# Optimization experiments

Hardware: AMD Instinct MI355X
Metric: run time of the kernel (lower is better)

## Reference

```python
import jax, jax.numpy as jnp
import numpy as np

N_NODES = 50000
N_EDGES = 800000
N_FEAT = 128
DIM = 32
N_GRAPHS = 500
N_CLASSES = 2


def setup_inputs() -> dict:
    key = jax.random.key(0)
    ks = jax.random.split(key, 10)
    x = jax.random.normal(ks[0], (N_NODES, N_FEAT), dtype=jnp.float32)
    edge_index = jax.random.randint(ks[1], (2, N_EDGES), 0, N_NODES, dtype=jnp.int64)
    batch = jnp.sort(jax.random.randint(ks[2], (N_NODES,), 0, N_GRAPHS, dtype=jnp.int64))
    edge_weight = jax.random.uniform(ks[3], (N_EDGES,), dtype=jnp.float32)
    s = 1.0 / np.sqrt(N_FEAT)
    w_rel = jax.random.uniform(ks[4], (N_FEAT, DIM), jnp.float32, -s, s)
    b_rel = jax.random.uniform(ks[5], (DIM,), jnp.float32, -s, s)
    w_root = jax.random.uniform(ks[6], (N_FEAT, DIM), jnp.float32, -s, s)
    s2 = 1.0 / np.sqrt(DIM)
    w_fc1 = jax.random.uniform(ks[7], (DIM, DIM), jnp.float32, -s2, s2)
    b_fc1 = jnp.zeros((DIM,), jnp.float32)
    w_fc2 = jax.random.uniform(ks[8], (DIM, N_CLASSES), jnp.float32, -s2, s2)
    b_fc2 = jnp.zeros((N_CLASSES,), jnp.float32)
    return {"x": x, "edge_weight": edge_weight, "w_rel": w_rel, "b_rel": b_rel,
            "w_root": w_root, "w_fc1": w_fc1, "b_fc1": b_fc1, "w_fc2": w_fc2,
            "b_fc2": b_fc2, "edge_index": edge_index, "batch": batch}


def reference(x, edge_weight, w_rel, b_rel, w_root, w_fc1, b_fc1, w_fc2, b_fc2,
              edge_index, batch):
    src, dst = edge_index[0], edge_index[1]
    # GraphConv: out_i = lin_rel(sum_{j->i} w_ji * x_j) + lin_root(x_i)
    msg = x[src] * edge_weight[:, None]                      # [E, F]
    agg = jax.ops.segment_sum(msg, dst, num_segments=N_NODES)  # [N, F]
    h = agg @ w_rel + b_rel + x @ w_root                     # [N, DIM]
    h = jax.nn.relu(h)
    # global_add_pool over graph ids
    pooled = jax.ops.segment_sum(h, batch, num_segments=N_GRAPHS)  # [G, DIM]
    h2 = jax.nn.relu(pooled @ w_fc1 + b_fc1)
    # dropout is identity in eval mode
    logits = h2 @ w_fc2 + b_fc2
    return jax.nn.log_softmax(logits, axis=-1)
```

## Files before the change

### kernel.cpp

```cpp
#include <hip/hip_runtime.h>

#define NN 50000
#define NE 800000
#define NF 128
#define DIM 32
#define NG 500
#define BK 32
#define NB ((NN + BK - 1) / BK)
#define PB 782
#define HB 128
#define CHUNK_E ((NE + HB - 1) / HB)
#define CAP 1024
#define SC7 7

typedef float  f32x4  __attribute__((ext_vector_type(4)));
typedef __bf16 bf16x8 __attribute__((ext_vector_type(8)));
typedef unsigned short u16x8 __attribute__((ext_vector_type(8)));

__device__ __forceinline__ unsigned rne16(float f) {
    unsigned u = __float_as_uint(f);
    return (u + 0x7FFFu + ((u >> 16) & 1u)) >> 16;
}
#define UIF __uint_as_float
__device__ __forceinline__ float blo(unsigned p) { return UIF(p << 16); }
__device__ __forceinline__ float bhi(unsigned p) { return UIF(p & 0xFFFF0000u); }

__global__ __launch_bounds__(256) void projhist_kernel(
    const float* __restrict__ x, const float* __restrict__ w_rel,
    const float* __restrict__ w_root, const float* __restrict__ b_rel,
    unsigned* __restrict__ yp, unsigned* __restrict__ rootp,
    const int* __restrict__ ei, int* __restrict__ H, float* __restrict__ pooled)
{
    __shared__ unsigned short s_wb[64 * 136];
    __shared__ float s_out[64 * 65];
    int tid = threadIdx.x;

    if (blockIdx.x >= PB) {
        int blk = blockIdx.x - PB;
        int* sh = (int*)s_wb;
        int pi = blk * 256 + tid;
        if (pi < NG * DIM) pooled[pi] = 0.0f;
        for (int i = tid; i < NB; i += 256) sh[i] = 0;
        __syncthreads();
        int base = blk * CHUNK_E;
        int end  = min(base + CHUNK_E, NE);
        for (int e = base + tid; e < end; e += 256)
            atomicAdd(&sh[ei[NE + e] >> 5], 1);
        __syncthreads();
        for (int i = tid; i < NB; i += 256) H[blk * NB + i] = sh[i];
        return;
    }

    for (int i = tid; i < 64 * NF; i += 256) {
        int k   = i >> 6;
        int col = i & 63;
        float v = (col < DIM) ? w_rel[k * DIM + col] : w_root[k * DIM + (col - DIM)];
        s_wb[col * 136 + k] = (unsigned short)rne16(v);
    }
    int rb = blockIdx.x * 64;
    __syncthreads();

    int l    = tid & 63;
    int w    = tid >> 6;
    int mrow = l & 15;
    int q    = l >> 4;
    int arow = min(rb + w * 16 + mrow, NN - 1);
    const float* xr = x + (size_t)arow * NF + q * 8;

    f32x4 acc0 = {0,0,0,0}, acc1 = {0,0,0,0}, acc2 = {0,0,0,0}, acc3 = {0,0,0,0};
#pragma unroll
    for (int k0 = 0; k0 < NF; k0 += 32) {
        float4 xa = *reinterpret_cast<const float4*>(xr + k0);
        float4 xb = *reinterpret_cast<const float4*>(xr + k0 + 4);
        u16x8 au;
        au[0] = (unsigned short)rne16(xa.x); au[1] = (unsigned short)rne16(xa.y);
        au[2] = (unsigned short)rne16(xa.z); au[3] = (unsigned short)rne16(xa.w);
        au[4] = (unsigned short)rne16(xb.x); au[5] = (unsigned short)rne16(xb.y);
        au[6] = (unsigned short)rne16(xb.z); au[7] = (unsigned short)rne16(xb.w);
        bf16x8 a = __builtin_bit_cast(bf16x8, au);
        int kb = k0 + q * 8;
        bf16x8 b0 = *reinterpret_cast<const bf16x8*>(&s_wb[(0  + mrow) * 136 + kb]);
        bf16x8 b1 = *reinterpret_cast<const bf16x8*>(&s_wb[(16 + mrow) * 136 + kb]);
        bf16x8 b2 = *reinterpret_cast<const bf16x8*>(&s_wb[(32 + mrow) * 136 + kb]);
        bf16x8 b3 = *reinterpret_cast<const bf16x8*>(&s_wb[(48 + mrow) * 136 + kb]);
        acc0 = __builtin_amdgcn_mfma_f32_16x16x32_bf16(a, b0, acc0, 0, 0, 0);
        acc1 = __builtin_amdgcn_mfma_f32_16x16x32_bf16(a, b1, acc1, 0, 0, 0);
        acc2 = __builtin_amdgcn_mfma_f32_16x16x32_bf16(a, b2, acc2, 0, 0, 0);
        acc3 = __builtin_amdgcn_mfma_f32_16x16x32_bf16(a, b3, acc3, 0, 0, 0);
    }
#pragma unroll
    for (int reg = 0; reg < 4; ++reg) {
        int srow = w * 16 + q * 4 + reg;
        s_out[srow * 65 +  0 + mrow] = acc0[reg];
        s_out[srow * 65 + 16 + mrow] = acc1[reg];
        s_out[srow * 65 + 32 + mrow] = acc2[reg];
        s_out[srow * 65 + 48 + mrow] = acc3[reg];
    }
    __syncthreads();

#pragma unroll
    for (int rep = 0; rep < 8; ++rep) {
        int idx = tid + rep * 256;
        int row = idx >> 5;
        int ui  = idx & 31;
        int n   = rb + row;
        if (n < NN) {
            if (ui < 16) {
                int c0 = ui * 2;
                unsigned p = rne16(s_out[row * 65 + c0]) |
                             (rne16(s_out[row * 65 + c0 + 1]) << 16);
                yp[(size_t)n * 16 + ui] = p;
            } else {
                int c0 = (ui - 16) * 2;
                float f0 = s_out[row * 65 + DIM + c0]     + b_rel[c0];
                float f1 = s_out[row * 65 + DIM + c0 + 1] + b_rel[c0 + 1];
                rootp[(size_t)n * 16 + (ui - 16)] = rne16(f0) | (rne16(f1) << 16);
            }
        }
    }
}

__global__ __launch_bounds__(256) void colscan(
    int* __restrict__ H, int* __restrict__ colsum)
{
    int b = blockIdx.x * 256 + threadIdx.x;
    if (b >= NB) return;
    int run = 0;
#pragma unroll 8
    for (int blk = 0; blk < HB; ++blk) {
        int v = H[blk * NB + b];
        H[blk * NB + b] = run;
        run += v;
    }
    colsum[b] = run;
}

__global__ __launch_bounds__(256) void partition_kernel(
    const int* __restrict__ ei, const float* __restrict__ ew,
    const int* __restrict__ H, const int* __restrict__ colsum,
    uint2* __restrict__ part, int* __restrict__ boff)
{
    __shared__ int s_scan[256];
    __shared__ int s_boff[NB + 1];
    __shared__ int cur[NB];
    int t = threadIdx.x;
    {
        int v[SC7]; int sum = 0;
#pragma unroll
        for (int j = 0; j < SC7; ++j) {
            int idx = t * SC7 + j;
            v[j] = (idx < NB) ? colsum[idx] : 0;
            sum += v[j];
        }
        s_scan[t] = sum;
        __syncthreads();
        for (int o = 1; o < 256; o <<= 1) {
            int u = (t >= o) ? s_scan[t - o] : 0;
            __syncthreads();
            s_scan[t] += u;
            __syncthreads();
        }
        int b2 = s_scan[t] - sum;
#pragma unroll
        for (int j = 0; j < SC7; ++j) {
            int idx = t * SC7 + j;
            if (idx < NB) { s_boff[idx] = b2; b2 += v[j]; }
        }
        if (t == 0) s_boff[NB] = NE;
        __syncthreads();
    }
    if (blockIdx.x == 0)
        for (int i = t; i <= NB; i += 256) boff[i] = s_boff[i];

    for (int i = t; i < NB; i += 256)
        cur[i] = s_boff[i] + H[blockIdx.x * NB + i];
    __syncthreads();
    int base = blockIdx.x * CHUNK_E;
    int end  = min(base + CHUNK_E, NE);
    for (int e = base + t; e < end; e += 256) {
        int s = ei[e], d = ei[NE + e];
        float w = ew[e];
        int b = d >> 5;
        int pos = atomicAdd(&cur[b], 1);
        part[pos] = make_uint2((unsigned)s | ((unsigned)(d & 31) << 16),
                               __float_as_uint(w));
    }
}

__global__ __launch_bounds__(256) void bucketagg_kernel(
    const uint2* __restrict__ ypq, const uint2* __restrict__ rootq,
    const uint2* __restrict__ part, const int* __restrict__ boff,
    const int* __restrict__ batch, float* __restrict__ pooled)
{
    __shared__ unsigned csr_lds[CAP];
    __shared__ int cnt[BK];
    __shared__ int cur[BK];
    __shared__ int off[BK + 1];
    int b = blockIdx.x, t = threadIdx.x;
    int s0 = boff[b], s1 = boff[b + 1], m = s1 - s0;

    uint2 rec[4];
    int nrec = 0;
    if (t < BK) cnt[t] = 0;
    __syncthreads();
#pragma unroll
    for (int i = 0; i < 4; ++i) {
        int idx = t + i * 256;
        if (idx < m) { rec[i] = part[s0 + idx]; nrec = i + 1; }
    }
#pragma unroll
    for (int i = 0; i < 4; ++i)
        if (i < nrec) atomicAdd(&cnt[rec[i].x >> 16], 1);
    __syncthreads();
    if (t < BK) {
        int v = cnt[t];
        int inc = v;
#pragma unroll
        for (int o = 1; o < BK; o <<= 1) {
            int u = __shfl_up(inc, o, 64);
            if (t >= o) inc += u;
        }
        off[t] = inc - v;
        cur[t] = inc - v;
        if (t == BK - 1) off[BK] = inc;
    }
    __syncthreads();
#pragma unroll
    for (int i = 0; i < 4; ++i)
        if (i < nrec) {
            uint2 pk = rec[i];
            int nl = pk.x >> 16;
            int pos = atomicAdd(&cur[nl], 1);
            csr_lds[pos] = (pk.x & 0xFFFFu) | (rne16(UIF(pk.y)) << 16);
        }
    if (t < BK) {
        int n = b * BK + t;
        cnt[t] = (n < NN) ? batch[n] : -1;
    }
    __syncthreads();

    int w    = t >> 6;
    int lane = t & 63;
    int g    = lane >> 3;
    int j    = lane & 7;
    int nl   = w * 8 + g;
    int n    = b * BK + nl;
    float v0 = 0, v1 = 0, v2 = 0, v3 = 0;
    if (n < NN) {
        int e  = off[nl];
        int e1 = off[nl + 1];
        for (; e + 4 <= e1; e += 4) {
            unsigned c0 = csr_lds[e],     c1 = csr_lds[e + 1];
            unsigned c2 = csr_lds[e + 2], c3 = csr_lds[e + 3];
            uint2 p0 = ypq[(c0 & 0xFFFFu) * 8 + j];
            uint2 p1 = ypq[(c1 & 0xFFFFu) * 8 + j];
            uint2 p2 = ypq[(c2 & 0xFFFFu) * 8 + j];
            uint2 p3 = ypq[(c3 & 0xFFFFu) * 8 + j];
            float w0 = UIF(c0 & 0xFFFF0000u), w1 = UIF(c1 & 0xFFFF0000u);
            float w2 = UIF(c2 & 0xFFFF0000u), w3 = UIF(c3 & 0xFFFF0000u);
            v0 = fmaf(w0, blo(p0.x), v0); v1 = fmaf(w0, bhi(p0.x), v1);
            v2 = fmaf(w0, blo(p0.y), v2); v3 = fmaf(w0, bhi(p0.y), v3);
            v0 = fmaf(w1, blo(p1.x), v0); v1 = fmaf(w1, bhi(p1.x), v1);
            v2 = fmaf(w1, blo(p1.y), v2); v3 = fmaf(w1, bhi(p1.y), v3);
            v0 = fmaf(w2, blo(p2.x), v0); v1 = fmaf(w2, bhi(p2.x), v1);
            v2 = fmaf(w2, blo(p2.y), v2); v3 = fmaf(w2, bhi(p2.y), v3);
            v0 = fmaf(w3, blo(p3.x), v0); v1 = fmaf(w3, bhi(p3.x), v1);
            v2 = fmaf(w3, blo(p3.y), v2); v3 = fmaf(w3, bhi(p3.y), v3);
        }
        for (; e < e1; ++e) {
            unsigned cu = csr_lds[e];
            uint2 p = ypq[(cu & 0xFFFFu) * 8 + j];
            float ww = UIF(cu & 0xFFFF0000u);
            v0 = fmaf(ww, blo(p.x), v0); v1 = fmaf(ww, bhi(p.x), v1);
            v2 = fmaf(ww, blo(p.y), v2); v3 = fmaf(ww, bhi(p.y), v3);
        }
        uint2 rr = rootq[(size_t)n * 8 + j];
        v0 = fmaxf(v0 + blo(rr.x), 0.0f);
        v1 = fmaxf(v1 + bhi(rr.x), 0.0f);
        v2 = fmaxf(v2 + blo(rr.y), 0.0f);
        v3 = fmaxf(v3 + bhi(rr.y), 0.0f);
    }
    __syncthreads();

    float* s_p = (float*)csr_lds;
    {
        float* dst = s_p + nl * DIM + 4 * j;
        dst[0] = v0; dst[1] = v1; dst[2] = v2; dst[3] = v3;
    }
    __syncthreads();

    int gi = t >> 5, c = t & 31;
    int rung = -1; float run = 0.0f;
#pragma unroll
    for (int k = 0; k < 4; ++k) {
        int nl2 = gi * 4 + k;
        int n2  = b * BK + nl2;
        if (n2 >= NN) break;
        float v = s_p[nl2 * DIM + c];
        int gg = cnt[nl2];
        if (gg != rung) {
            if (rung >= 0) atomicAdd(&pooled[rung * DIM + c], run);
            rung = gg; run = v;
        } else run += v;
    }
    if (rung >= 0) atomicAdd(&pooled[rung * DIM + c], run);
}

__global__ __launch_bounds__(512) void head_kernel(
    const float* __restrict__ pooled, const float* __restrict__ w_fc1,
    const float* __restrict__ b_fc1, const float* __restrict__ w_fc2,
    const float* __restrict__ b_fc2, float* __restrict__ out)
{
    __shared__ float s_fc1[DIM * DIM];
    __shared__ float s_b1[DIM];
    __shared__ float s_fc2[DIM * 2];
    __shared__ float s_b2[2];
    int tid = threadIdx.x;
    s_fc1[tid]       = w_fc1[tid];
    s_fc1[tid + 512] = w_fc1[tid + 512];
    if (tid < DIM * 2) s_fc2[tid] = w_fc2[tid];
    if (tid < DIM)     s_b1[tid]  = b_fc1[tid];
    if (tid < 2)       s_b2[tid]  = b_fc2[tid];
    __syncthreads();

    int g = tid;
    if (g >= NG) return;
    const float* p = pooled + g * DIM;
    float h2[DIM];
#pragma unroll
    for (int c = 0; c < DIM; ++c) {
        float a = s_b1[c];
#pragma unroll
        for (int k = 0; k < DIM; ++k)
            a = fmaf(p[k], s_fc1[k * DIM + c], a);
        h2[c] = a > 0.0f ? a : 0.0f;
    }
    float l0 = s_b2[0], l1 = s_b2[1];
#pragma unroll
    for (int c = 0; c < DIM; ++c) {
        l0 = fmaf(h2[c], s_fc2[c * 2 + 0], l0);
        l1 = fmaf(h2[c], s_fc2[c * 2 + 1], l1);
    }
    float m   = fmaxf(l0, l1);
    float lse = m + logf(expf(l0 - m) + expf(l1 - m));
    out[g * 2 + 0] = l0 - lse;
    out[g * 2 + 1] = l1 - lse;
}

extern "C" void kernel_launch(void* const* d_in, const int* in_sizes, int n_in,
                              void* d_out, int out_size, void* d_ws, size_t ws_size,
                              hipStream_t stream) {
    const float* x      = (const float*)d_in[0];
    const float* ew     = (const float*)d_in[1];
    const float* w_rel  = (const float*)d_in[2];
    const float* b_rel  = (const float*)d_in[3];
    const float* w_root = (const float*)d_in[4];
    const float* w_fc1  = (const float*)d_in[5];
    const float* b_fc1  = (const float*)d_in[6];
    const float* w_fc2  = (const float*)d_in[7];
    const float* b_fc2  = (const float*)d_in[8];
    const int*   ei     = (const int*)d_in[9];
    const int*   batch  = (const int*)d_in[10];
    float* out = (float*)d_out;

    char* ws = (char*)d_ws;
    unsigned* yp    = (unsigned*)ws;
    unsigned* rootp = yp + (size_t)NN * 16;
    uint2* part     = (uint2*)(rootp + (size_t)NN * 16);
    int*   H        = (int*)(part + NE);
    int*   colsum   = H + (size_t)HB * NB;
    int*   boff     = colsum + NB;
    float* pooled   = (float*)(boff + NB + 2);

    projhist_kernel<<<PB + HB, 256, 0, stream>>>(x, w_rel, w_root, b_rel,
                                                 yp, rootp, ei, H, pooled);
    colscan<<<(NB + 255) / 256, 256, 0, stream>>>(H, colsum);
    partition_kernel<<<HB, 256, 0, stream>>>(ei, ew, H, colsum, part, boff);
    bucketagg_kernel<<<NB, 256, 0, stream>>>((const uint2*)yp, (const uint2*)rootp,
                                             part, boff, batch, pooled);
    head_kernel<<<1, 512, 0, stream>>>(pooled, w_fc1, b_fc1, w_fc2, b_fc2, out);
}
```

Measured before the change: 66.99 us.

## Fuse MLP head into bucket aggregation via last-block ticket; unroll gather by 8

Removes the separate head kernel launch. The last bucketagg block to finish, found with an atomic ticket counter that projhist resets, now runs the FC1/FC2/log-softmax head after a threadfence, staging the head weights in an enlarged LDS buffer. The edge gather loop is also unrolled from 4 to 8 to keep more independent loads in flight. The costs are a serialized tail on one 256-thread block, higher LDS and register use, and reliance on the threadfence/ticket pattern for correct ordering of the atomics.

```diff
diff --git a/kernel.cpp b/kernel.cpp
--- a/kernel.cpp
+++ b/kernel.cpp
@@ -11,6 +11,7 @@
 #define HB 128
 #define CHUNK_E ((NE + HB - 1) / HB)
 #define CAP 1024
+#define LDSW 1184
 #define SC7 7
 
 typedef float  f32x4  __attribute__((ext_vector_type(4)));
@@ -29,7 +30,8 @@
     const float* __restrict__ x, const float* __restrict__ w_rel,
     const float* __restrict__ w_root, const float* __restrict__ b_rel,
     unsigned* __restrict__ yp, unsigned* __restrict__ rootp,
-    const int* __restrict__ ei, int* __restrict__ H, float* __restrict__ pooled)
+    const int* __restrict__ ei, int* __restrict__ H, float* __restrict__ pooled,
+    int* __restrict__ done_cnt)
 {
     __shared__ unsigned short s_wb[64 * 136];
     __shared__ float s_out[64 * 65];
@@ -38,6 +40,7 @@
     if (blockIdx.x >= PB) {
         int blk = blockIdx.x - PB;
         int* sh = (int*)s_wb;
+        if (blk == 0 && tid == 0) *done_cnt = 0;
         int pi = blk * 256 + tid;
         if (pi < NG * DIM) pooled[pi] = 0.0f;
         for (int i = tid; i < NB; i += 256) sh[i] = 0;
@@ -190,12 +193,17 @@
 __global__ __launch_bounds__(256) void bucketagg_kernel(
     const uint2* __restrict__ ypq, const uint2* __restrict__ rootq,
     const uint2* __restrict__ part, const int* __restrict__ boff,
-    const int* __restrict__ batch, float* __restrict__ pooled)
+    const int* __restrict__ batch, float* __restrict__ pooled,
+    int* __restrict__ done_cnt,
+    const float* __restrict__ w_fc1, const float* __restrict__ b_fc1,
+    const float* __restrict__ w_fc2, const float* __restrict__ b_fc2,
+    float* __restrict__ out)
 {
-    __shared__ unsigned csr_lds[CAP];
+    __shared__ unsigned csr_lds[LDSW];
     __shared__ int cnt[BK];
     __shared__ int cur[BK];
     __shared__ int off[BK + 1];
+    __shared__ int s_last;
     int b = blockIdx.x, t = threadIdx.x;
     int s0 = boff[b], s1 = boff[b + 1], m = s1 - s0;
 
@@ -249,15 +257,23 @@
     if (n < NN) {
         int e  = off[nl];
         int e1 = off[nl + 1];
-        for (; e + 4 <= e1; e += 4) {
+        for (; e + 8 <= e1; e += 8) {
             unsigned c0 = csr_lds[e],     c1 = csr_lds[e + 1];
             unsigned c2 = csr_lds[e + 2], c3 = csr_lds[e + 3];
+            unsigned c4 = csr_lds[e + 4], c5 = csr_lds[e + 5];
+            unsigned c6 = csr_lds[e + 6], c7 = csr_lds[e + 7];
             uint2 p0 = ypq[(c0 & 0xFFFFu) * 8 + j];
             uint2 p1 = ypq[(c1 & 0xFFFFu) * 8 + j];
             uint2 p2 = ypq[(c2 & 0xFFFFu) * 8 + j];
             uint2 p3 = ypq[(c3 & 0xFFFFu) * 8 + j];
+            uint2 p4 = ypq[(c4 & 0xFFFFu) * 8 + j];
+            uint2 p5 = ypq[(c5 & 0xFFFFu) * 8 + j];
+            uint2 p6 = ypq[(c6 & 0xFFFFu) * 8 + j];
+            uint2 p7 = ypq[(c7 & 0xFFFFu) * 8 + j];
             float w0 = UIF(c0 & 0xFFFF0000u), w1 = UIF(c1 & 0xFFFF0000u);
             float w2 = UIF(c2 & 0xFFFF0000u), w3 = UIF(c3 & 0xFFFF0000u);
+            float w4 = UIF(c4 & 0xFFFF0000u), w5 = UIF(c5 & 0xFFFF0000u);
+            float w6 = UIF(c6 & 0xFFFF0000u), w7 = UIF(c7 & 0xFFFF0000u);
             v0 = fmaf(w0, blo(p0.x), v0); v1 = fmaf(w0, bhi(p0.x), v1);
             v2 = fmaf(w0, blo(p0.y), v2); v3 = fmaf(w0, bhi(p0.y), v3);
             v0 = fmaf(w1, blo(p1.x), v0); v1 = fmaf(w1, bhi(p1.x), v1);
@@ -266,6 +282,14 @@
             v2 = fmaf(w2, blo(p2.y), v2); v3 = fmaf(w2, bhi(p2.y), v3);
             v0 = fmaf(w3, blo(p3.x), v0); v1 = fmaf(w3, bhi(p3.x), v1);
             v2 = fmaf(w3, blo(p3.y), v2); v3 = fmaf(w3, bhi(p3.y), v3);
+            v0 = fmaf(w4, blo(p4.x), v0); v1 = fmaf(w4, bhi(p4.x), v1);
+            v2 = fmaf(w4, blo(p4.y), v2); v3 = fmaf(w4, bhi(p4.y), v3);
+            v0 = fmaf(w5, blo(p5.x), v0); v1 = fmaf(w5, bhi(p5.x), v1);
+            v2 = fmaf(w5, blo(p5.y), v2); v3 = fmaf(w5, bhi(p5.y), v3);
+            v0 = fmaf(w6, blo(p6.x), v0); v1 = fmaf(w6, bhi(p6.x), v1);
+            v2 = fmaf(w6, blo(p6.y), v2); v3 = fmaf(w6, bhi(p6.y), v3);
+            v0 = fmaf(w7, blo(p7.x), v0); v1 = fmaf(w7, bhi(p7.x), v1);
+            v2 = fmaf(w7, blo(p7.y), v2); v3 = fmaf(w7, bhi(p7.y), v3);
         }
         for (; e < e1; ++e) {
             unsigned cu = csr_lds[e];
@@ -304,47 +328,46 @@
         } else run += v;
     }
     if (rung >= 0) atomicAdd(&pooled[rung * DIM + c], run);
-}
-
-__global__ __launch_bounds__(512) void head_kernel(
-    const float* __restrict__ pooled, const float* __restrict__ w_fc1,
-    const float* __restrict__ b_fc1, const float* __restrict__ w_fc2,
-    const float* __restrict__ b_fc2, float* __restrict__ out)
-{
-    __shared__ float s_fc1[DIM * DIM];
-    __shared__ float s_b1[DIM];
-    __shared__ float s_fc2[DIM * 2];
-    __shared__ float s_b2[2];
-    int tid = threadIdx.x;
-    s_fc1[tid]       = w_fc1[tid];
-    s_fc1[tid + 512] = w_fc1[tid + 512];
-    if (tid < DIM * 2) s_fc2[tid] = w_fc2[tid];
-    if (tid < DIM)     s_b1[tid]  = b_fc1[tid];
-    if (tid < 2)       s_b2[tid]  = b_fc2[tid];
-    __syncthreads();
-
-    int g = tid;
-    if (g >= NG) return;
-    const float* p = pooled + g * DIM;
-    float h2[DIM];
-#pragma unroll
-    for (int c = 0; c < DIM; ++c) {
-        float a = s_b1[c];
+
+    __threadfence();
+    __syncthreads();
+    if (t == 0) {
+        int ticket = atomicAdd(done_cnt, 1);
+        s_last = (ticket == (int)gridDim.x - 1) ? 1 : 0;
+    }
+    __syncthreads();
+    if (!s_last) return;
+
+    float* sf = (float*)csr_lds;
+    sf[t] = w_fc1[t]; sf[256 + t] = w_fc1[256 + t];
+    sf[512 + t] = w_fc1[512 + t]; sf[768 + t] = w_fc1[768 + t];
+    if (t < DIM)     sf[1024 + t] = b_fc1[t];
+    if (t < DIM * 2) sf[1056 + t] = w_fc2[t];
+    if (t < 2)       sf[1120 + t] = b_fc2[t];
+    __syncthreads();
+
+    for (int gq = t; gq < NG; gq += 256) {
+        float pv[DIM];
 #pragma unroll
         for (int k = 0; k < DIM; ++k)
-            a = fmaf(p[k], s_fc1[k * DIM + c], a);
-        h2[c] = a > 0.0f ? a : 0.0f;
-    }
-    float l0 = s_b2[0], l1 = s_b2[1];
-#pragma unroll
-    for (int c = 0; c < DIM; ++c) {
-        l0 = fmaf(h2[c], s_fc2[c * 2 + 0], l0);
-        l1 = fmaf(h2[c], s_fc2[c * 2 + 1], l1);
-    }
-    float m   = fmaxf(l0, l1);
-    float lse = m + logf(expf(l0 - m) + expf(l1 - m));
-    out[g * 2 + 0] = l0 - lse;
-    out[g * 2 + 1] = l1 - lse;
+            pv[k] = __hip_atomic_load(&pooled[gq * DIM + k],
+                                      __ATOMIC_RELAXED, __HIP_MEMORY_SCOPE_AGENT);
+        float l0 = sf[1120], l1 = sf[1121];
+#pragma unroll 1
+        for (int cc = 0; cc < DIM; ++cc) {
+            float a = sf[1024 + cc];
+#pragma unroll
+            for (int k = 0; k < DIM; ++k)
+                a = fmaf(pv[k], sf[k * DIM + cc], a);
+            a = fmaxf(a, 0.0f);
+            l0 = fmaf(a, sf[1056 + cc * 2 + 0], l0);
+            l1 = fmaf(a, sf[1056 + cc * 2 + 1], l1);
+        }
+        float mm  = fmaxf(l0, l1);
+        float lse = mm + logf(expf(l0 - mm) + expf(l1 - mm));
+        out[gq * 2 + 0] = l0 - lse;
+        out[gq * 2 + 1] = l1 - lse;
+    }
 }
 
 extern "C" void kernel_launch(void* const* d_in, const int* in_sizes, int n_in,
@@ -370,13 +393,14 @@
     int*   H        = (int*)(part + NE);
     int*   colsum   = H + (size_t)HB * NB;
     int*   boff     = colsum + NB;
-    float* pooled   = (float*)(boff + NB + 2);
+    int*   done_cnt = boff + NB + 2;
+    float* pooled   = (float*)(done_cnt + 2);
 
     projhist_kernel<<<PB + HB, 256, 0, stream>>>(x, w_rel, w_root, b_rel,
-                                                 yp, rootp, ei, H, pooled);
+                                                 yp, rootp, ei, H, pooled, done_cnt);
     colscan<<<(NB + 255) / 256, 256, 0, stream>>>(H, colsum);
     partition_kernel<<<HB, 256, 0, stream>>>(ei, ew, H, colsum, part, boff);
     bucketagg_kernel<<<NB, 256, 0, stream>>>((const uint2*)yp, (const uint2*)rootp,
-                                             part, boff, batch, pooled);
-    head_kernel<<<1, 512, 0, stream>>>(pooled, w_fc1, b_fc1, w_fc2, b_fc2, out);
-}
+                                             part, boff, batch, pooled, done_cnt,
+                                             w_fc1, b_fc1, w_fc2, b_fc2, out);
+}
```

After: 173.8 us. 159% more time.

## Balance bucket aggregation across edges and interleave histogram chunk order

Applied to the files above, without the earlier changes.

The per-bucket aggregation now splits the bucket's edge list evenly across the four waves instead of giving each 8-lane group one destination node. Each group walks a strided slice of edges, keeps a running sum per destination node, and flushes it into a shared-memory accumulator with LDS atomics when the node changes. Root add and ReLU are applied afterwards from that accumulator. This targets load imbalance from uneven node degrees, at the cost of extra LDS atomics, an extra shared buffer and a node-id array. Separately, the histogram and partition blocks remap their block index to an interleaved edge-chunk row, which changes which chunks run concurrently.

```diff
diff --git a/kernel.cpp b/kernel.cpp
--- a/kernel.cpp
+++ b/kernel.cpp
@@ -37,17 +37,18 @@
 
     if (blockIdx.x >= PB) {
         int blk = blockIdx.x - PB;
+        int row = ((blk & 7) << 4) | (blk >> 3);
         int* sh = (int*)s_wb;
         int pi = blk * 256 + tid;
         if (pi < NG * DIM) pooled[pi] = 0.0f;
         for (int i = tid; i < NB; i += 256) sh[i] = 0;
         __syncthreads();
-        int base = blk * CHUNK_E;
+        int base = row * CHUNK_E;
         int end  = min(base + CHUNK_E, NE);
         for (int e = base + tid; e < end; e += 256)
             atomicAdd(&sh[ei[NE + e] >> 5], 1);
         __syncthreads();
-        for (int i = tid; i < NB; i += 256) H[blk * NB + i] = sh[i];
+        for (int i = tid; i < NB; i += 256) H[row * NB + i] = sh[i];
         return;
     }
 
@@ -144,6 +145,7 @@
     __shared__ int s_boff[NB + 1];
     __shared__ int cur[NB];
     int t = threadIdx.x;
+    int row = ((blockIdx.x & 7) << 4) | (blockIdx.x >> 3);
     {
         int v[SC7]; int sum = 0;
 #pragma unroll
@@ -173,9 +175,9 @@
         for (int i = t; i <= NB; i += 256) boff[i] = s_boff[i];
 
     for (int i = t; i < NB; i += 256)
-        cur[i] = s_boff[i] + H[blockIdx.x * NB + i];
-    __syncthreads();
-    int base = blockIdx.x * CHUNK_E;
+        cur[i] = s_boff[i] + H[row * NB + i];
+    __syncthreads();
+    int base = row * CHUNK_E;
     int end  = min(base + CHUNK_E, NE);
     for (int e = base + t; e < end; e += 256) {
         int s = ei[e], d = ei[NE + e];
@@ -193,16 +195,21 @@
     const int* __restrict__ batch, float* __restrict__ pooled)
 {
     __shared__ unsigned csr_lds[CAP];
+    __shared__ unsigned char nid[CAP];
+    __shared__ float accf[BK * DIM];
     __shared__ int cnt[BK];
     __shared__ int cur[BK];
     __shared__ int off[BK + 1];
     int b = blockIdx.x, t = threadIdx.x;
     int s0 = boff[b], s1 = boff[b + 1], m = s1 - s0;
 
+    if (t < BK) cnt[t] = 0;
+#pragma unroll
+    for (int i = 0; i < BK * DIM / 256; ++i) accf[t + i * 256] = 0.0f;
+    __syncthreads();
+
     uint2 rec[4];
     int nrec = 0;
-    if (t < BK) cnt[t] = 0;
-    __syncthreads();
 #pragma unroll
     for (int i = 0; i < 4; ++i) {
         int idx = t + i * 256;
@@ -232,6 +239,7 @@
             int nl = pk.x >> 16;
             int pos = atomicAdd(&cur[nl], 1);
             csr_lds[pos] = (pk.x & 0xFFFFu) | (rne16(UIF(pk.y)) << 16);
+            nid[pos] = (unsigned char)nl;
         }
     if (t < BK) {
         int n = b * BK + t;
@@ -243,49 +251,60 @@
     int lane = t & 63;
     int g    = lane >> 3;
     int j    = lane & 7;
-    int nl   = w * 8 + g;
-    int n    = b * BK + nl;
+    int per  = (m + 3) >> 2;
+    int qs   = w * per;
+    int qe   = min(qs + per, m);
+
     float v0 = 0, v1 = 0, v2 = 0, v3 = 0;
-    if (n < NN) {
-        int e  = off[nl];
-        int e1 = off[nl + 1];
-        for (; e + 4 <= e1; e += 4) {
-            unsigned c0 = csr_lds[e],     c1 = csr_lds[e + 1];
-            unsigned c2 = csr_lds[e + 2], c3 = csr_lds[e + 3];
-            uint2 p0 = ypq[(c0 & 0xFFFFu) * 8 + j];
-            uint2 p1 = ypq[(c1 & 0xFFFFu) * 8 + j];
-            uint2 p2 = ypq[(c2 & 0xFFFFu) * 8 + j];
-            uint2 p3 = ypq[(c3 & 0xFFFFu) * 8 + j];
-            float w0 = UIF(c0 & 0xFFFF0000u), w1 = UIF(c1 & 0xFFFF0000u);
-            float w2 = UIF(c2 & 0xFFFF0000u), w3 = UIF(c3 & 0xFFFF0000u);
-            v0 = fmaf(w0, blo(p0.x), v0); v1 = fmaf(w0, bhi(p0.x), v1);
-            v2 = fmaf(w0, blo(p0.y), v2); v3 = fmaf(w0, bhi(p0.y), v3);
-            v0 = fmaf(w1, blo(p1.x), v0); v1 = fmaf(w1, bhi(p1.x), v1);
-            v2 = fmaf(w1, blo(p1.y), v2); v3 = fmaf(w1, bhi(p1.y), v3);
-            v0 = fmaf(w2, blo(p2.x), v0); v1 = fmaf(w2, bhi(p2.x), v1);
-            v2 = fmaf(w2, blo(p2.y), v2); v3 = fmaf(w2, bhi(p2.y), v3);
-            v0 = fmaf(w3, blo(p3.x), v0); v1 = fmaf(w3, bhi(p3.x), v1);
-            v2 = fmaf(w3, blo(p3.y), v2); v3 = fmaf(w3, bhi(p3.y), v3);
-        }
-        for (; e < e1; ++e) {
-            unsigned cu = csr_lds[e];
-            uint2 p = ypq[(cu & 0xFFFFu) * 8 + j];
-            float ww = UIF(cu & 0xFFFF0000u);
-            v0 = fmaf(ww, blo(p.x), v0); v1 = fmaf(ww, bhi(p.x), v1);
-            v2 = fmaf(ww, blo(p.y), v2); v3 = fmaf(ww, bhi(p.y), v3);
-        }
-        uint2 rr = rootq[(size_t)n * 8 + j];
-        v0 = fmaxf(v0 + blo(rr.x), 0.0f);
-        v1 = fmaxf(v1 + bhi(rr.x), 0.0f);
-        v2 = fmaxf(v2 + blo(rr.y), 0.0f);
-        v3 = fmaxf(v3 + bhi(rr.y), 0.0f);
-    }
-    __syncthreads();
-
-    float* s_p = (float*)csr_lds;
+    int cur3 = -1;
+
+#define FLUSH() { \
+    atomicAdd(&accf[cur3 * DIM + 4 * j + 0], v0); \
+    atomicAdd(&accf[cur3 * DIM + 4 * j + 1], v1); \
+    atomicAdd(&accf[cur3 * DIM + 4 * j + 2], v2); \
+    atomicAdd(&accf[cur3 * DIM + 4 * j + 3], v3); }
+#define PROC(cu, ne, p) { \
+    if (ne != cur3) { \
+        if (cur3 >= 0) FLUSH(); \
+        cur3 = ne; v0 = v1 = v2 = v3 = 0.0f; } \
+    float ww = UIF((cu) & 0xFFFF0000u); \
+    v0 = fmaf(ww, blo((p).x), v0); v1 = fmaf(ww, bhi((p).x), v1); \
+    v2 = fmaf(ww, blo((p).y), v2); v3 = fmaf(ww, bhi((p).y), v3); }
+
+    int e = qs + g;
+    for (; e + 24 < qe; e += 32) {
+        unsigned c0 = csr_lds[e],      c1 = csr_lds[e + 8];
+        unsigned c2 = csr_lds[e + 16], c3 = csr_lds[e + 24];
+        int n0 = nid[e], n1 = nid[e + 8], n2 = nid[e + 16], n3 = nid[e + 24];
+        uint2 p0 = ypq[(c0 & 0xFFFFu) * 8 + j];
+        uint2 p1 = ypq[(c1 & 0xFFFFu) * 8 + j];
+        uint2 p2 = ypq[(c2 & 0xFFFFu) * 8 + j];
+        uint2 p3 = ypq[(c3 & 0xFFFFu) * 8 + j];
+        PROC(c0, n0, p0); PROC(c1, n1, p1);
+        PROC(c2, n2, p2); PROC(c3, n3, p3);
+    }
+    for (; e < qe; e += 8) {
+        unsigned cu = csr_lds[e];
+        int ne = nid[e];
+        uint2 p = ypq[(cu & 0xFFFFu) * 8 + j];
+        PROC(cu, ne, p);
+    }
+    if (cur3 >= 0) FLUSH();
+#undef PROC
+#undef FLUSH
+    __syncthreads();
+
     {
-        float* dst = s_p + nl * DIM + 4 * j;
-        dst[0] = v0; dst[1] = v1; dst[2] = v2; dst[3] = v3;
+        int nl2 = t >> 3, j2 = t & 7;
+        int n2  = b * BK + nl2;
+        if (n2 < NN) {
+            uint2 rr = rootq[(size_t)n2 * 8 + j2];
+            float* ap = accf + nl2 * DIM + 4 * j2;
+            ap[0] = fmaxf(ap[0] + blo(rr.x), 0.0f);
+            ap[1] = fmaxf(ap[1] + bhi(rr.x), 0.0f);
+            ap[2] = fmaxf(ap[2] + blo(rr.y), 0.0f);
+            ap[3] = fmaxf(ap[3] + bhi(rr.y), 0.0f);
+        }
     }
     __syncthreads();
 
@@ -296,7 +315,7 @@
         int nl2 = gi * 4 + k;
         int n2  = b * BK + nl2;
         if (n2 >= NN) break;
-        float v = s_p[nl2 * DIM + c];
+        float v = accf[nl2 * DIM + c];
         int gg = cnt[nl2];
         if (gg != rung) {
             if (rung >= 0) atomicAdd(&pooled[rung * DIM + c], run);
```

Result: slower. 133.2 us (+98.9%).
